# Kernel optimization log

Hardware: AMD Instinct MI355X
Metric: run time of the kernel (lower is better)

## Reference

```python
import jax, jax.numpy as jnp
import numpy as np

N_NODES = 50000
N_EDGES = 800000
IN_CH = 64
HID = 64
EDGE_DIM = 16


def _glorot(key, shape):
    fan_in, fan_out = shape[0], shape[1]
    lim = (6.0 / (fan_in + fan_out)) ** 0.5
    return jax.random.uniform(key, shape, jnp.float32, -lim, lim)


def setup_inputs() -> dict:
    key = jax.random.key(0)
    ks = jax.random.split(key, 12)
    x = jax.random.normal(ks[0], (N_NODES, IN_CH), jnp.float32)
    edge_index = jax.random.randint(ks[1], (2, N_EDGES), 0, N_NODES, jnp.int64)
    edge_attr = jax.random.normal(ks[2], (N_EDGES, EDGE_DIM), jnp.float32)
    # SAGEConv1: lin_l (aggregated neighbors, with bias) + lin_r (root, no bias)
    W1l = _glorot(ks[3], (IN_CH, HID)); b1l = jnp.zeros((HID,), jnp.float32)
    W1r = _glorot(ks[4], (IN_CH, HID))
    # SAGEConv2
    W2l = _glorot(ks[5], (HID, HID)); b2l = jnp.zeros((HID,), jnp.float32)
    W2r = _glorot(ks[6], (HID, HID))
    # edge MLP: Linear(2*HID+EDGE_DIM -> HID), ReLU, Linear(HID -> 1)
    Wm1 = _glorot(ks[7], (2 * HID + EDGE_DIM, HID))
    bm1 = jnp.zeros((HID,), jnp.float32)
    Wm2 = _glorot(ks[8], (HID, 1))
    bm2 = jnp.zeros((1,), jnp.float32)
    return dict(x=x, edge_index=edge_index, edge_attr=edge_attr,
                W1l=W1l, b1l=b1l, W1r=W1r,
                W2l=W2l, b2l=b2l, W2r=W2r,
                Wm1=Wm1, bm1=bm1, Wm2=Wm2, bm2=bm2)


def _sage_conv(x, src, dst, deg_inv, Wl, bl, Wr):
    # mean aggregation of source-node features at destination nodes
    n = x.shape[0]
    agg = jax.ops.segment_sum(x[src], dst, num_segments=n)  # [N, d]
    agg = agg * deg_inv  # mean over incoming edges
    return agg @ Wl + bl + x @ Wr


def reference(x, edge_index, edge_attr, W1l, b1l, W1r, W2l, b2l, W2r, Wm1, bm1, Wm2, bm2):
    src, dst = edge_index[0], edge_index[1]
    n = x.shape[0]
    # in-degree (over dst), clamped to 1 as in PyG mean aggregation
    deg = jax.ops.segment_sum(jnp.ones((src.shape[0],), x.dtype), dst, num_segments=n)
    deg_inv = (1.0 / jnp.maximum(deg, 1.0))[:, None]  # [N,1]

    h = jax.nn.relu(_sage_conv(x, src, dst, deg_inv, W1l, b1l, W1r))
    h = jax.nn.relu(_sage_conv(h, src, dst, deg_inv, W2l, b2l, W2r))

    # gather endpoint embeddings + concat with edge features -> MLP score
    edge_input = jnp.concatenate([h[src], h[dst], edge_attr], axis=-1)  # [E, 2H+De]
    hidden = jax.nn.relu(edge_input @ Wm1 + bm1)
    return (hidden @ Wm2 + bm2).squeeze(-1)  # [E]
```

## Files before the change

kernel.cpp:

```cpp
#include <hip/hip_runtime.h>
#include <hip/hip_bf16.h>


#define C 64
#define KP 168
#define SK 136
#define TILE_E 64

typedef short short8 __attribute__((ext_vector_type(8)));
typedef float f32x4 __attribute__((ext_vector_type(4)));

__device__ __forceinline__ unsigned short f2bf(float f) {
    unsigned int u = __float_as_uint(f);
    return (unsigned short)((u + 0x7FFFu + ((u >> 16) & 1u)) >> 16);
}
__device__ __forceinline__ unsigned int pack2(float lo, float hi) {
    return (unsigned int)f2bf(lo) | ((unsigned int)f2bf(hi) << 16);
}
__device__ __forceinline__ float bflo(unsigned int u) { return __uint_as_float(u << 16); }
__device__ __forceinline__ float bfhi(unsigned int u) { return __uint_as_float(u & 0xFFFF0000u); }

__global__ void deg_count_int(const int* __restrict__ dst, int* __restrict__ degi, int E) {
    int e = blockIdx.x * blockDim.x + threadIdx.x;
    if (e < E) atomicAdd(&degi[dst[e]], 1);
}

__global__ __launch_bounds__(256) void scan_partial(const int* __restrict__ degi,
        int* __restrict__ rowptr, int* __restrict__ partials, int N) {
    __shared__ int sWs[4];
    int t = threadIdx.x, b = blockIdx.x;
    int g0 = b * 1024 + t * 4;
    int v0 = (g0 + 0 < N) ? degi[g0 + 0] : 0;
    int v1 = (g0 + 1 < N) ? degi[g0 + 1] : 0;
    int v2 = (g0 + 2 < N) ? degi[g0 + 2] : 0;
    int v3 = (g0 + 3 < N) ? degi[g0 + 3] : 0;
    int tsum = v0 + v1 + v2 + v3;
    int lane = t & 63, w = t >> 6;
    int incl = tsum;
    #pragma unroll
    for (int m = 1; m < 64; m <<= 1) {
        int y = __shfl_up(incl, m, 64);
        if (lane >= m) incl += y;
    }
    if (lane == 63) sWs[w] = incl;
    __syncthreads();
    int wprefix = 0;
    for (int i = 0; i < w; ++i) wprefix += sWs[i];
    int run = wprefix + incl - tsum;
    if (g0 + 0 < N) rowptr[g0 + 0] = run; run += v0;
    if (g0 + 1 < N) rowptr[g0 + 1] = run; run += v1;
    if (g0 + 2 < N) rowptr[g0 + 2] = run; run += v2;
    if (g0 + 3 < N) rowptr[g0 + 3] = run;
    if (t == 255) partials[b] = wprefix + incl;
}

__global__ void scan_offsets(const int* __restrict__ partials, int* __restrict__ offsets, int nb) {
    int lane = threadIdx.x;
    int v = (lane < nb) ? partials[lane] : 0;
    int incl = v;
    #pragma unroll
    for (int m = 1; m < 64; m <<= 1) {
        int y = __shfl_up(incl, m, 64);
        if (lane >= m) incl += y;
    }
    if (lane < nb) offsets[lane] = incl - v;
}

__global__ void scan_add(int* __restrict__ rowptr, const int* __restrict__ offsets,
                         int* __restrict__ cursor, const int* __restrict__ degi,
                         float* __restrict__ deg_inv, int N, int E) {
    int i = blockIdx.x * blockDim.x + threadIdx.x;
    if (i < N) {
        int r = rowptr[i] + offsets[i >> 10];
        rowptr[i] = r;
        cursor[i] = r;
        deg_inv[i] = 1.0f / fmaxf((float)degi[i], 1.0f);
    }
    if (i == 0) rowptr[N] = E;
}

__global__ void fill_csr(const int* __restrict__ src, const int* __restrict__ dst,
                         int* __restrict__ cursor, int* __restrict__ eSrc, int E) {
    int e = blockIdx.x * blockDim.x + threadIdx.x;
    if (e < E) {
        int p = atomicAdd(&cursor[dst[e]], 1);
        eSrc[p] = src[e];
    }
}

__global__ void to_bf16(const float* __restrict__ in, unsigned short* __restrict__ outb, int n8) {
    int i = blockIdx.x * blockDim.x + threadIdx.x;
    if (i >= n8) return;
    const float4* p = (const float4*)(in + (size_t)i * 8);
    float4 a = p[0], b = p[1];
    uint4 o;
    o.x = pack2(a.x, a.y); o.y = pack2(a.z, a.w);
    o.z = pack2(b.x, b.y); o.w = pack2(b.z, b.w);
    *(uint4*)(outb + (size_t)i * 8) = o;
}

__global__ __launch_bounds__(256) void csr_agg_bf16(const unsigned short* __restrict__ fB,
        const int* __restrict__ rowptr, const int* __restrict__ eSrc,
        const float* __restrict__ deg_inv, unsigned short* __restrict__ aggB, int N) {
    int node = blockIdx.x * 4 + (threadIdx.x >> 6);
    if (node >= N) return;
    int lane = threadIdx.x & 63;
    int s8 = lane >> 3, ci = lane & 7;
    int row = rowptr[node], end = rowptr[node + 1];
    float a[8] = {0.f, 0.f, 0.f, 0.f, 0.f, 0.f, 0.f, 0.f};
    for (int j0 = row; j0 < end; j0 += 8) {
        int j = j0 + s8;
        if (j < end) {
            int s = eSrc[j];
            uint4 v = *(const uint4*)(fB + (size_t)s * C + ci * 8);
            a[0] += bflo(v.x); a[1] += bfhi(v.x);
            a[2] += bflo(v.y); a[3] += bfhi(v.y);
            a[4] += bflo(v.z); a[5] += bfhi(v.z);
            a[6] += bflo(v.w); a[7] += bfhi(v.w);
        }
    }
    #pragma unroll
    for (int m = 8; m < 64; m <<= 1)
        #pragma unroll
        for (int k = 0; k < 8; ++k)
            a[k] += __shfl_xor(a[k], m, 64);
    if (s8 == 0) {
        float di = deg_inv[node];
        uint4 o;
        o.x = pack2(a[0] * di, a[1] * di);
        o.y = pack2(a[2] * di, a[3] * di);
        o.z = pack2(a[4] * di, a[5] * di);
        o.w = pack2(a[6] * di, a[7] * di);
        *(uint4*)(aggB + (size_t)node * C + ci * 8) = o;
    }
}

__global__ __launch_bounds__(256) void dense_mfma(
        const unsigned short* __restrict__ aB, const unsigned short* __restrict__ xB,
        const float* __restrict__ Wl, const float* __restrict__ Wr,
        const float* __restrict__ bl, unsigned short* __restrict__ hOut, int N) {
    __shared__ unsigned short sW[C * SK];
    __shared__ unsigned short sAB[C * SK];
    int t = threadIdx.x;
    int lane = t & 63, w = t >> 6;
    int l15 = lane & 15, quad = lane >> 4;
    int n0 = blockIdx.x * 64;

    for (int i = t; i < 128 * C; i += 256) {
        int k = i >> 6, n = i & 63;
        float v = (k < C) ? Wl[k * C + n] : Wr[(k - C) * C + n];
        sW[n * SK + k] = f2bf(v);
    }
    for (int i = t; i < 64 * 16; i += 256) {
        int r = i >> 4, ch = i & 15;
        int node = n0 + r;
        uint4 v = {0u, 0u, 0u, 0u};
        if (node < N)
            v = (ch < 8) ? *(const uint4*)(aB + (size_t)node * C + ch * 8)
                         : *(const uint4*)(xB + (size_t)node * C + (ch - 8) * 8);
        *(uint4*)&sAB[r * SK + ch * 8] = v;
    }
    __syncthreads();

    short8 bW[4][4];
    #pragma unroll
    for (int t4 = 0; t4 < 4; ++t4)
        #pragma unroll
        for (int kc = 0; kc < 4; ++kc)
            bW[t4][kc] = *(const short8*)&sW[(t4 * 16 + l15) * SK + kc * 32 + quad * 8];
    float blr[4];
    #pragma unroll
    for (int t4 = 0; t4 < 4; ++t4) blr[t4] = bl[t4 * 16 + l15];

    f32x4 acc[4] = {{0.f, 0.f, 0.f, 0.f}, {0.f, 0.f, 0.f, 0.f},
                    {0.f, 0.f, 0.f, 0.f}, {0.f, 0.f, 0.f, 0.f}};
    #pragma unroll
    for (int kc = 0; kc < 4; ++kc) {
        short8 a = *(const short8*)&sAB[(w * 16 + l15) * SK + kc * 32 + quad * 8];
        #pragma unroll
        for (int t4 = 0; t4 < 4; ++t4)
            acc[t4] = __builtin_amdgcn_mfma_f32_16x16x32_bf16(a, bW[t4][kc], acc[t4], 0, 0, 0);
    }
    __syncthreads();

    #pragma unroll
    for (int t4 = 0; t4 < 4; ++t4)
        #pragma unroll
        for (int r = 0; r < 4; ++r) {
            int rl = w * 16 + quad * 4 + r;
            sW[rl * 72 + t4 * 16 + l15] = f2bf(fmaxf(acc[t4][r] + blr[t4], 0.f));
        }
    __syncthreads();
    for (int i = t; i < 64 * 8; i += 256) {
        int r = i >> 3, c8 = i & 7;
        int node = n0 + r;
        if (node < N)
            *(uint4*)(hOut + (size_t)node * C + c8 * 8) = *(const uint4*)&sW[r * 72 + c8 * 8];
    }
}

__global__ __launch_bounds__(256) void edge_mlp_reg(
        const unsigned short* __restrict__ hB, const int* __restrict__ src,
        const int* __restrict__ dst, const float* __restrict__ ea,
        const float* __restrict__ Wm1, const float* __restrict__ bm1,
        const float* __restrict__ Wm2, const float* __restrict__ bm2,
        float* __restrict__ out, int E, int nTiles) {
    __shared__ unsigned short sW[C * KP];
    int t = threadIdx.x;
    int lane = t & 63, w = t >> 6;
    int l15 = lane & 15, quad = lane >> 4;

    for (int i = t; i < C * 3; i += 256) {
        int r = i / 3, cc = 144 + (i % 3) * 8;
        uint4 z = {0u, 0u, 0u, 0u};
        *(uint4*)&sW[r * KP + cc] = z;
    }
    for (int i = t; i < 144 * C; i += 256) {
        int k = i >> 6, n = i & 63;
        sW[n * KP + k] = f2bf(Wm1[i]);
    }
    __syncthreads();

    short8 bW[4][5];
    #pragma unroll
    for (int t4 = 0; t4 < 4; ++t4)
        #pragma unroll
        for (int kc = 0; kc < 5; ++kc)
            bW[t4][kc] = *(const short8*)&sW[(t4 * 16 + l15) * KP + kc * 32 + quad * 8];
    float bmr[4], w2r[4];
    #pragma unroll
    for (int t4 = 0; t4 < 4; ++t4) {
        int j = t4 * 16 + l15;
        bmr[t4] = bm1[j];
        w2r[t4] = Wm2[j];
    }
    float bb = bm2[0];

    for (int tile = blockIdx.x; tile < nTiles; tile += gridDim.x) {
        int e0 = tile * TILE_E;
        int idx = e0 + w * 16 + l15;
        int idxc = (idx < E) ? idx : 0;
        int s = src[idxc], d = dst[idxc];

        const uint4* ps = (const uint4*)(hB + (size_t)s * C);
        const uint4* pd = (const uint4*)(hB + (size_t)d * C);
        uint4 u0 = ps[quad];
        uint4 u1 = ps[4 + quad];
        uint4 u2 = pd[quad];
        uint4 u3 = pd[4 + quad];
        uint4 u4 = {0u, 0u, 0u, 0u};
        if (quad < 2) {
            const float4* pe = (const float4*)(ea + (size_t)idxc * 16 + quad * 8);
            float4 f0 = pe[0], f1 = pe[1];
            u4.x = pack2(f0.x, f0.y); u4.y = pack2(f0.z, f0.w);
            u4.z = pack2(f1.x, f1.y); u4.w = pack2(f1.z, f1.w);
        }
        short8 a0 = *(short8*)&u0, a1 = *(short8*)&u1, a2 = *(short8*)&u2,
               a3 = *(short8*)&u3, a4 = *(short8*)&u4;

        f32x4 acc[4] = {{0.f, 0.f, 0.f, 0.f}, {0.f, 0.f, 0.f, 0.f},
                        {0.f, 0.f, 0.f, 0.f}, {0.f, 0.f, 0.f, 0.f}};
        #pragma unroll
        for (int t4 = 0; t4 < 4; ++t4) {
            acc[t4] = __builtin_amdgcn_mfma_f32_16x16x32_bf16(a0, bW[t4][0], acc[t4], 0, 0, 0);
            acc[t4] = __builtin_amdgcn_mfma_f32_16x16x32_bf16(a1, bW[t4][1], acc[t4], 0, 0, 0);
            acc[t4] = __builtin_amdgcn_mfma_f32_16x16x32_bf16(a2, bW[t4][2], acc[t4], 0, 0, 0);
            acc[t4] = __builtin_amdgcn_mfma_f32_16x16x32_bf16(a3, bW[t4][3], acc[t4], 0, 0, 0);
            acc[t4] = __builtin_amdgcn_mfma_f32_16x16x32_bf16(a4, bW[t4][4], acc[t4], 0, 0, 0);
        }

        float sres[4];
        #pragma unroll
        for (int r = 0; r < 4; ++r) {
            float v = 0.f;
            #pragma unroll
            for (int t4 = 0; t4 < 4; ++t4)
                v += fmaxf(acc[t4][r] + bmr[t4], 0.f) * w2r[t4];
            #pragma unroll
            for (int m = 1; m < 16; m <<= 1)
                v += __shfl_xor(v, m, 16);
            sres[r] = v;
        }
        if (l15 == 0) {
            #pragma unroll
            for (int r = 0; r < 4; ++r) {
                int e = e0 + w * 16 + quad * 4 + r;
                if (e < E) out[e] = sres[r] + bb;
            }
        }
    }
}

extern "C" void kernel_launch(void* const* d_in, const int* in_sizes, int n_in,
                              void* d_out, int out_size, void* d_ws, size_t ws_size,
                              hipStream_t stream) {
    const float* x   = (const float*)d_in[0];
    const int*   ei  = (const int*)d_in[1];
    const float* ea  = (const float*)d_in[2];
    const float* W1l = (const float*)d_in[3];
    const float* b1l = (const float*)d_in[4];
    const float* W1r = (const float*)d_in[5];
    const float* W2l = (const float*)d_in[6];
    const float* b2l = (const float*)d_in[7];
    const float* W2r = (const float*)d_in[8];
    const float* Wm1 = (const float*)d_in[9];
    const float* bm1 = (const float*)d_in[10];
    const float* Wm2 = (const float*)d_in[11];
    const float* bm2 = (const float*)d_in[12];
    float* out = (float*)d_out;

    const int N = in_sizes[0] / C;
    const int E = in_sizes[1] / 2;
    const int* src = ei;
    const int* dst = ei + E;

    char* wsb = (char*)d_ws;
    int npad = (N + 1023) & ~1023;
    float* deg_inv = (float*)wsb;               wsb += (size_t)npad * 4;
    unsigned short* xB   = (unsigned short*)wsb; wsb += (size_t)npad * C * 2;
    unsigned short* h1B  = (unsigned short*)wsb; wsb += (size_t)npad * C * 2;
    unsigned short* h2B  = (unsigned short*)wsb; wsb += (size_t)npad * C * 2;
    unsigned short* aggB = (unsigned short*)wsb; wsb += (size_t)npad * C * 2;
    int* degi    = (int*)wsb;                   wsb += (size_t)npad * 4;
    int* rowptr  = (int*)wsb;                   wsb += (size_t)(npad + 64) * 4;
    int* cursor  = (int*)wsb;                   wsb += (size_t)npad * 4;
    int* eSrc    = (int*)wsb;                   wsb += (size_t)E * 4;
    int* partials = (int*)wsb;                  wsb += 64 * 4;
    int* offsets  = (int*)wsb;

    int tpb = 256;
    int nb = (N + 1023) / 1024;

    hipMemsetAsync(degi, 0, (size_t)N * sizeof(int), stream);
    deg_count_int<<<(E + tpb - 1) / tpb, tpb, 0, stream>>>(dst, degi, E);
    to_bf16<<<((N * C / 8) + tpb - 1) / tpb, tpb, 0, stream>>>(x, xB, N * C / 8);
    scan_partial<<<nb, tpb, 0, stream>>>(degi, rowptr, partials, N);
    scan_offsets<<<1, 64, 0, stream>>>(partials, offsets, nb);
    scan_add<<<(N + tpb - 1) / tpb, tpb, 0, stream>>>(rowptr, offsets, cursor, degi, deg_inv, N, E);
    fill_csr<<<(E + tpb - 1) / tpb, tpb, 0, stream>>>(src, dst, cursor, eSrc, E);

    csr_agg_bf16<<<(N + 3) / 4, tpb, 0, stream>>>(xB, rowptr, eSrc, deg_inv, aggB, N);
    dense_mfma<<<(N + 63) / 64, tpb, 0, stream>>>(aggB, xB, W1l, W1r, b1l, h1B, N);

    csr_agg_bf16<<<(N + 3) / 4, tpb, 0, stream>>>(h1B, rowptr, eSrc, deg_inv, aggB, N);
    dense_mfma<<<(N + 63) / 64, tpb, 0, stream>>>(aggB, h1B, W2l, W2r, b2l, h2B, N);

    int nTiles = (E + TILE_E - 1) / TILE_E;
    int grid = nTiles < 2048 ? nTiles : 2048;
    edge_mlp_reg<<<grid, tpb, 0, stream>>>(h2B, src, dst, ea, Wm1, bm1, Wm2, bm2, out, E, nTiles);
}
```

Before: 320.1 us.

## Prefetch next edge tile in MLP, unroll CSR gather, pre-convert edge attrs

The edge MLP kernel now software-pipelines its grid-stride loop: it loads indices two tiles ahead and gathers node rows one tile ahead, so gather latency overlaps with MFMA compute. The CSR aggregation loop is unrolled to issue two independent row gathers per iteration. Edge attributes are converted to bf16 inside the degree-count kernel when workspace allows, so the MLP reads half as many bytes for them. This adds an extra pass over edge_attr and more registers held for prefetched rows.

Result: no change. 314.9 us (-1.6%).

```diff
diff --git a/kernel.cpp b/kernel.cpp
--- a/kernel.cpp
+++ b/kernel.cpp
@@ -20,9 +20,19 @@
 __device__ __forceinline__ float bflo(unsigned int u) { return __uint_as_float(u << 16); }
 __device__ __forceinline__ float bfhi(unsigned int u) { return __uint_as_float(u & 0xFFFF0000u); }
 
-__global__ void deg_count_int(const int* __restrict__ dst, int* __restrict__ degi, int E) {
-    int e = blockIdx.x * blockDim.x + threadIdx.x;
-    if (e < E) atomicAdd(&degi[dst[e]], 1);
+__global__ void deg_count_ea(const int* __restrict__ dst, int* __restrict__ degi,
+                             const float* __restrict__ ea, unsigned short* __restrict__ eaB,
+                             int E, int doEa) {
+    int i = blockIdx.x * blockDim.x + threadIdx.x;
+    if (i < E) atomicAdd(&degi[dst[i]], 1);
+    if (doEa && i < 2 * E) {
+        const float4* p = (const float4*)(ea + (size_t)i * 8);
+        float4 a = p[0], b = p[1];
+        uint4 o;
+        o.x = pack2(a.x, a.y); o.y = pack2(a.z, a.w);
+        o.z = pack2(b.x, b.y); o.w = pack2(b.z, b.w);
+        *(uint4*)(eaB + (size_t)i * 8) = o;
+    }
 }
 
 __global__ __launch_bounds__(256) void scan_partial(const int* __restrict__ degi,
@@ -108,10 +118,24 @@
     int s8 = lane >> 3, ci = lane & 7;
     int row = rowptr[node], end = rowptr[node + 1];
     float a[8] = {0.f, 0.f, 0.f, 0.f, 0.f, 0.f, 0.f, 0.f};
-    for (int j0 = row; j0 < end; j0 += 8) {
-        int j = j0 + s8;
-        if (j < end) {
-            int s = eSrc[j];
+    int j = row;
+    for (; j + 16 <= end; j += 16) {
+        int sA = eSrc[j + s8];
+        int sB = eSrc[j + 8 + s8];
+        uint4 vA = *(const uint4*)(fB + (size_t)sA * C + ci * 8);
+        uint4 vB = *(const uint4*)(fB + (size_t)sB * C + ci * 8);
+        a[0] += bflo(vA.x); a[1] += bfhi(vA.x);
+        a[2] += bflo(vA.y); a[3] += bfhi(vA.y);
+        a[4] += bflo(vA.z); a[5] += bfhi(vA.z);
+        a[6] += bflo(vA.w); a[7] += bfhi(vA.w);
+        a[0] += bflo(vB.x); a[1] += bfhi(vB.x);
+        a[2] += bflo(vB.y); a[3] += bfhi(vB.y);
+        a[4] += bflo(vB.z); a[5] += bfhi(vB.z);
+        a[6] += bflo(vB.w); a[7] += bfhi(vB.w);
+    }
+    for (; j < end; j += 8) {
+        if (j + s8 < end) {
+            int s = eSrc[j + s8];
             uint4 v = *(const uint4*)(fB + (size_t)s * C + ci * 8);
             a[0] += bflo(v.x); a[1] += bfhi(v.x);
             a[2] += bflo(v.y); a[3] += bfhi(v.y);
@@ -199,9 +223,35 @@
     }
 }
 
-__global__ __launch_bounds__(256) void edge_mlp_reg(
+template <bool EAB>
+__device__ __forceinline__ void gather_rows(const unsigned short* __restrict__ hB,
+        const unsigned short* __restrict__ eaB, const float* __restrict__ ea,
+        int s, int d, int idxc, int quad,
+        uint4& u0, uint4& u1, uint4& u2, uint4& u3, uint4& u4) {
+    const uint4* ps = (const uint4*)(hB + (size_t)s * C);
+    const uint4* pd = (const uint4*)(hB + (size_t)d * C);
+    u0 = ps[quad];
+    u1 = ps[4 + quad];
+    u2 = pd[quad];
+    u3 = pd[4 + quad];
+    u4.x = 0u; u4.y = 0u; u4.z = 0u; u4.w = 0u;
+    if (quad < 2) {
+        if (EAB) {
+            u4 = *(const uint4*)(eaB + (size_t)idxc * 16 + quad * 8);
+        } else {
+            const float4* pe = (const float4*)(ea + (size_t)idxc * 16 + quad * 8);
+            float4 f0 = pe[0], f1 = pe[1];
+            u4.x = pack2(f0.x, f0.y); u4.y = pack2(f0.z, f0.w);
+            u4.z = pack2(f1.x, f1.y); u4.w = pack2(f1.z, f1.w);
+        }
+    }
+}
+
+template <bool EAB>
+__global__ __launch_bounds__(256) void edge_mlp_pipe(
         const unsigned short* __restrict__ hB, const int* __restrict__ src,
         const int* __restrict__ dst, const float* __restrict__ ea,
+        const unsigned short* __restrict__ eaB,
         const float* __restrict__ Wm1, const float* __restrict__ bm1,
         const float* __restrict__ Wm2, const float* __restrict__ bm2,
         float* __restrict__ out, int E, int nTiles) {
@@ -236,28 +286,28 @@
     }
     float bb = bm2[0];
 
-    for (int tile = blockIdx.x; tile < nTiles; tile += gridDim.x) {
-        int e0 = tile * TILE_E;
-        int idx = e0 + w * 16 + l15;
-        int idxc = (idx < E) ? idx : 0;
-        int s = src[idxc], d = dst[idxc];
-
-        const uint4* ps = (const uint4*)(hB + (size_t)s * C);
-        const uint4* pd = (const uint4*)(hB + (size_t)d * C);
-        uint4 u0 = ps[quad];
-        uint4 u1 = ps[4 + quad];
-        uint4 u2 = pd[quad];
-        uint4 u3 = pd[4 + quad];
-        uint4 u4 = {0u, 0u, 0u, 0u};
-        if (quad < 2) {
-            const float4* pe = (const float4*)(ea + (size_t)idxc * 16 + quad * 8);
-            float4 f0 = pe[0], f1 = pe[1];
-            u4.x = pack2(f0.x, f0.y); u4.y = pack2(f0.z, f0.w);
-            u4.z = pack2(f1.x, f1.y); u4.w = pack2(f1.z, f1.w);
-        }
-        short8 a0 = *(short8*)&u0, a1 = *(short8*)&u1, a2 = *(short8*)&u2,
-               a3 = *(short8*)&u3, a4 = *(short8*)&u4;
-
+    int stride = gridDim.x;
+    int lbase = w * 16 + l15;
+
+    int tile = blockIdx.x;
+    int idxc = min(tile * TILE_E + lbase, E - 1);
+    int s = src[idxc], d = dst[idxc];
+    int tileN = tile + stride;
+    int idxNc = (tileN < nTiles) ? min(tileN * TILE_E + lbase, E - 1) : idxc;
+    int sN = src[idxNc], dN = dst[idxNc];
+    uint4 cu0, cu1, cu2, cu3, cu4;
+    gather_rows<EAB>(hB, eaB, ea, s, d, idxc, quad, cu0, cu1, cu2, cu3, cu4);
+
+    while (true) {
+        bool hasNext = (tileN < nTiles);
+        uint4 nu0, nu1, nu2, nu3, nu4;
+        gather_rows<EAB>(hB, eaB, ea, sN, dN, idxNc, quad, nu0, nu1, nu2, nu3, nu4);
+        int tileNN = tileN + stride;
+        int idxNNc = (tileNN < nTiles) ? min(tileNN * TILE_E + lbase, E - 1) : idxNc;
+        int sNN = src[idxNNc], dNN = dst[idxNNc];
+
+        short8 a0 = *(short8*)&cu0, a1 = *(short8*)&cu1, a2 = *(short8*)&cu2,
+               a3 = *(short8*)&cu3, a4 = *(short8*)&cu4;
         f32x4 acc[4] = {{0.f, 0.f, 0.f, 0.f}, {0.f, 0.f, 0.f, 0.f},
                         {0.f, 0.f, 0.f, 0.f}, {0.f, 0.f, 0.f, 0.f}};
         #pragma unroll
@@ -282,12 +332,19 @@
             sres[r] = v;
         }
         if (l15 == 0) {
+            int e0 = tile * TILE_E;
             #pragma unroll
             for (int r = 0; r < 4; ++r) {
                 int e = e0 + w * 16 + quad * 4 + r;
                 if (e < E) out[e] = sres[r] + bb;
             }
         }
+
+        if (!hasNext) break;
+        tile = tileN; tileN = tileNN;
+        idxc = idxNc; idxNc = idxNNc;
+        s = sN; sN = sNN; d = dN; dN = dNN;
+        cu0 = nu0; cu1 = nu1; cu2 = nu2; cu3 = nu3; cu4 = nu4;
     }
 }
 
@@ -316,23 +373,26 @@
 
     char* wsb = (char*)d_ws;
     int npad = (N + 1023) & ~1023;
-    float* deg_inv = (float*)wsb;               wsb += (size_t)npad * 4;
+    float* deg_inv = (float*)wsb;                wsb += (size_t)npad * 4;
     unsigned short* xB   = (unsigned short*)wsb; wsb += (size_t)npad * C * 2;
     unsigned short* h1B  = (unsigned short*)wsb; wsb += (size_t)npad * C * 2;
     unsigned short* h2B  = (unsigned short*)wsb; wsb += (size_t)npad * C * 2;
     unsigned short* aggB = (unsigned short*)wsb; wsb += (size_t)npad * C * 2;
-    int* degi    = (int*)wsb;                   wsb += (size_t)npad * 4;
-    int* rowptr  = (int*)wsb;                   wsb += (size_t)(npad + 64) * 4;
-    int* cursor  = (int*)wsb;                   wsb += (size_t)npad * 4;
-    int* eSrc    = (int*)wsb;                   wsb += (size_t)E * 4;
-    int* partials = (int*)wsb;                  wsb += 64 * 4;
-    int* offsets  = (int*)wsb;
+    int* degi    = (int*)wsb;                    wsb += (size_t)npad * 4;
+    int* rowptr  = (int*)wsb;                    wsb += (size_t)(npad + 64) * 4;
+    int* cursor  = (int*)wsb;                    wsb += (size_t)npad * 4;
+    int* eSrc    = (int*)wsb;                    wsb += (size_t)E * 4;
+    int* partials = (int*)wsb;                   wsb += 64 * 4;
+    int* offsets  = (int*)wsb;                   wsb += 64 * 4;
+    unsigned short* eaB = (unsigned short*)wsb;
+    size_t used = (size_t)(wsb - (char*)d_ws);
+    int useEaB = (ws_size >= used + (size_t)E * 16 * 2) ? 1 : 0;
 
     int tpb = 256;
     int nb = (N + 1023) / 1024;
 
     hipMemsetAsync(degi, 0, (size_t)N * sizeof(int), stream);
-    deg_count_int<<<(E + tpb - 1) / tpb, tpb, 0, stream>>>(dst, degi, E);
+    deg_count_ea<<<(2 * E + tpb - 1) / tpb, tpb, 0, stream>>>(dst, degi, ea, eaB, E, useEaB);
     to_bf16<<<((N * C / 8) + tpb - 1) / tpb, tpb, 0, stream>>>(x, xB, N * C / 8);
     scan_partial<<<nb, tpb, 0, stream>>>(degi, rowptr, partials, N);
     scan_offsets<<<1, 64, 0, stream>>>(partials, offsets, nb);
@@ -347,5 +407,10 @@
 
     int nTiles = (E + TILE_E - 1) / TILE_E;
     int grid = nTiles < 2048 ? nTiles : 2048;
-    edge_mlp_reg<<<grid, tpb, 0, stream>>>(h2B, src, dst, ea, Wm1, bm1, Wm2, bm2, out, E, nTiles);
-}
+    if (useEaB)
+        edge_mlp_pipe<true><<<grid, tpb, 0, stream>>>(h2B, src, dst, ea, eaB,
+                Wm1, bm1, Wm2, bm2, out, E, nTiles);
+    else
+        edge_mlp_pipe<false><<<grid, tpb, 0, stream>>>(h2B, src, dst, ea, eaB,
+                Wm1, bm1, Wm2, bm2, out, E, nTiles);
+}
```
